# Kernel tuning notes

Measured on AMD Instinct MI355X. Metric: run time of the kernel, lower is better.

## Reference

```python
import jax, jax.numpy as jnp
import numpy as np

N = 10000
E = 160000
H = 8
C = 128
D = 1024
NB = 3
NG = 64
NEG_SLOPE = 0.2
BN_EPS = 1e-5


def setup_inputs() -> dict:
    key = jax.random.key(0)
    ks = jax.random.split(key, 12)
    x = jax.random.normal(ks[0], (N, D), dtype=jnp.float32)
    edge_index = jax.random.randint(ks[1], (2, E), 0, N, dtype=jnp.int64)
    batch = jnp.sort(jax.random.randint(ks[2], (N,), 0, NG, dtype=jnp.int64))
    W = jax.random.normal(ks[3], (NB, D, D), dtype=jnp.float32) * 0.03
    att_src = jax.random.normal(ks[4], (NB, H, C), dtype=jnp.float32) * 0.1
    att_dst = jax.random.normal(ks[5], (NB, H, C), dtype=jnp.float32) * 0.1
    att_bias = jnp.zeros((NB, D), dtype=jnp.float32)
    gamma = jnp.ones((NB, D), dtype=jnp.float32)
    beta = jnp.zeros((NB, D), dtype=jnp.float32)
    W_out = jax.random.normal(ks[6], (D, 2), dtype=jnp.float32) * 0.03
    b_out = jnp.zeros((2,), dtype=jnp.float32)
    return {"x": x, "edge_index": edge_index, "batch": batch, "W": W,
            "att_src": att_src, "att_dst": att_dst, "att_bias": att_bias,
            "gamma": gamma, "beta": beta, "W_out": W_out, "b_out": b_out}


def _gat_conv(x, Wb, a_src, a_dst, bias, src, dst):
    # linear projection, per-head view: [N, H, C]
    h = (x @ Wb).reshape(N, H, C)
    alpha_src = jnp.einsum('nhc,hc->nh', h, a_src)  # [N,H]
    alpha_dst = jnp.einsum('nhc,hc->nh', h, a_dst)
    e = jax.nn.leaky_relu(alpha_src[src] + alpha_dst[dst], NEG_SLOPE)  # [Etot,H]
    # segment softmax over incoming edges per destination node
    m = jax.ops.segment_max(e, dst, num_segments=N)  # every node has self-loop
    ex = jnp.exp(e - m[dst])
    denom = jax.ops.segment_sum(ex, dst, num_segments=N)
    alpha = ex / denom[dst]  # [Etot,H]
    msg = alpha[:, :, None] * h[src]  # [Etot,H,C]
    out = jax.ops.segment_sum(msg, dst, num_segments=N).reshape(N, H * C)
    return out + bias


def _batchnorm(x, g, b):
    mu = jnp.mean(x, axis=0)
    var = jnp.mean(jnp.square(x - mu), axis=0)  # biased, training mode
    return (x - mu) * jax.lax.rsqrt(var + BN_EPS) * g + b


def reference(x, edge_index, batch, W, att_src, att_dst, att_bias, gamma, beta, W_out, b_out):
    # add self loops (PyG GATConv default)
    loop = jnp.arange(N, dtype=edge_index.dtype)
    src = jnp.concatenate([edge_index[0], loop])
    dst = jnp.concatenate([edge_index[1], loop])

    h = x
    prev = x
    for i in range(NB):
        att = _gat_conv(h, W[i], att_src[i], att_dst[i], att_bias[i], src, dst)
        o = jax.nn.relu(_batchnorm(prev + att, gamma[i], beta[i]))
        prev = h
        h = o

    # global mean pool over graphs
    sums = jax.ops.segment_sum(h, batch, num_segments=NG)
    cnts = jax.ops.segment_sum(jnp.ones((N,), dtype=h.dtype), batch, num_segments=NG)
    pooled = sums / jnp.maximum(cnts, 1.0)[:, None]
    return pooled @ W_out + b_out
```

## Files before the change

### kernel.cpp

```cpp
#include <hip/hip_runtime.h>
#include <hip/hip_bf16.h>

#define N_NODES 10000
#define E_EDGES 160000
#define ETOT    170000
#define H_HEADS 8
#define C_CH    128
#define D_DIM   1024
#define NBLK    3
#define NGRAPH  64
#define NEG_SLOPE 0.2f
#define BN_EPS  1e-5f

typedef __attribute__((ext_vector_type(8))) _Float16 half8;
typedef __attribute__((ext_vector_type(4))) _Float16 half4;
typedef __attribute__((ext_vector_type(2))) _Float16 half2v;
typedef __attribute__((ext_vector_type(4))) float f32x4;

__device__ inline int lower_bound_batch(const int* __restrict__ batch, int g) {
    int lo = 0, hi = N_NODES;
    while (lo < hi) {
        int mid = (lo + hi) >> 1;
        if (batch[mid] < g) lo = mid + 1;
        else hi = mid;
    }
    return lo;
}

__global__ void deg_kernel(const int* __restrict__ ei, int* __restrict__ deg) {
    int tid = blockIdx.x * blockDim.x + threadIdx.x;
    if (tid >= ETOT) return;
    int dst = (tid < E_EDGES) ? ei[E_EDGES + tid] : (tid - E_EDGES);
    atomicAdd(&deg[dst], 1);
}

__global__ void scan_kernel(const int* __restrict__ deg, int* __restrict__ ioff) {
    __shared__ int part[256];
    int t = threadIdx.x;
    const int CH = (N_NODES + 255) / 256;
    int base = t * CH;
    int s = 0;
    for (int j = 0; j < CH; ++j) {
        int idx = base + j;
        if (idx < N_NODES) s += deg[idx];
    }
    part[t] = s;
    __syncthreads();
    for (int o = 1; o < 256; o <<= 1) {
        int v = 0;
        if (t >= o) v = part[t - o];
        __syncthreads();
        part[t] += v;
        __syncthreads();
    }
    int run = (t == 0) ? 0 : part[t - 1];
    for (int j = 0; j < CH; ++j) {
        int idx = base + j;
        if (idx < N_NODES) { ioff[idx] = run; run += deg[idx]; }
    }
}

__global__ void scatter_kernel(const int* __restrict__ ei, int* __restrict__ ioff,
                               int* __restrict__ csr_src) {
    int tid = blockIdx.x * blockDim.x + threadIdx.x;
    if (tid >= ETOT) return;
    int src, dst;
    if (tid < E_EDGES) { src = ei[tid]; dst = ei[E_EDGES + tid]; }
    else { src = dst = tid - E_EDGES; }
    int pos = atomicAdd(&ioff[dst], 1);
    csr_src[pos] = src;
}

__global__ __launch_bounds__(256) void xconv_kernel(const float* __restrict__ in,
                                                    _Float16* __restrict__ o, int n4) {
    int i = blockIdx.x * blockDim.x + threadIdx.x;
    if (i >= n4) return;
    float4 v = ((const float4*)in)[i];
    half4 h = {(_Float16)v.x, (_Float16)v.y, (_Float16)v.z, (_Float16)v.w};
    ((half4*)o)[i] = h;
}

__global__ __launch_bounds__(256) void wtconv_kernel(const float* __restrict__ Wall,
                                                     _Float16* __restrict__ t16all) {
    const float* W = Wall + (size_t)blockIdx.z * D_DIM * D_DIM;
    _Float16* t16 = t16all + (size_t)blockIdx.z * D_DIM * D_DIM;
    __shared__ float t[32][33];
    int bn = blockIdx.x * 32;
    int bk = blockIdx.y * 32;
    int tx = threadIdx.x & 31;
    int ty = threadIdx.x >> 5;
#pragma unroll
    for (int r = 0; r < 32; r += 8)
        t[ty + r][tx] = W[(size_t)(bk + ty + r) * D_DIM + bn + tx];
    __syncthreads();
#pragma unroll
    for (int r = 0; r < 32; r += 8)
        t16[(size_t)(bn + ty + r) * D_DIM + bk + tx] = (_Float16)t[tx][ty + r];
}

__global__ __launch_bounds__(256, 4) void gemm_mfma_kernel(const _Float16* __restrict__ A,
                                                           const _Float16* __restrict__ Bt,
                                                           _Float16* __restrict__ Hout,
                                                           const float* __restrict__ att_s,
                                                           const float* __restrict__ att_d,
                                                           float* __restrict__ asrc,
                                                           float* __restrict__ adst,
                                                           float* __restrict__ stats, int M) {
    __shared__ short As[128 * 64];
    __shared__ short Bs[64 * 64];
    int bx = blockIdx.x;
    int tid = threadIdx.x;
    if (bx == 0) {
#pragma unroll
        for (int j = 0; j < 8; ++j) stats[tid + j * 256] = 0.f;
    }
    int c = bx & 7;
    int nt = (bx >> 3) & 15;
    int mt = c + 8 * (bx >> 7);
    if (mt >= 79) return;
    int bm = mt * 128;
    int head = nt >> 1;
    int bncol = (nt & 1) * 64;
    int bnrow = nt * 64;
    int wave = tid >> 6;
    int lane = tid & 63;
    int wm = wave * 32;
    int quad = lane >> 4;
    int l16 = lane & 15;

    f32x4 acc[2][4];
#pragma unroll
    for (int i = 0; i < 2; ++i)
#pragma unroll
        for (int j = 0; j < 4; ++j) acc[i][j] = (f32x4){0.f, 0.f, 0.f, 0.f};

    int srow8 = lane >> 3;
    int sswz = ((lane & 7) ^ srow8) << 4;
    const char* gA[4];
    const char* gB[2];
    char* ldA[4];
    char* ldB[2];
#pragma unroll
    for (int r = 0; r < 4; ++r) {
        int arow = wave * 8 + r * 32 + srow8;
        int ga = bm + arow;
        if (ga > M - 1) ga = M - 1;
        gA[r] = (const char*)(A + (size_t)ga * 1024) + sswz;
        ldA[r] = (char*)As + (wave * 8 + r * 32) * 128;
    }
#pragma unroll
    for (int r = 0; r < 2; ++r) {
        int brow = wave * 8 + r * 32 + srow8;
        gB[r] = (const char*)(Bt + (size_t)(bnrow + brow) * 1024) + sswz;
        ldB[r] = (char*)Bs + (wave * 8 + r * 32) * 128;
    }

    int xr = l16 & 7;
    for (int kb = 0; kb < 16; ++kb) {
        int ko = kb * 128;
#pragma unroll
        for (int r = 0; r < 4; ++r)
            __builtin_amdgcn_global_load_lds(
                (const __attribute__((address_space(1))) void*)(gA[r] + ko),
                (__attribute__((address_space(3))) void*)ldA[r], 16, 0, 0);
#pragma unroll
        for (int r = 0; r < 2; ++r)
            __builtin_amdgcn_global_load_lds(
                (const __attribute__((address_space(1))) void*)(gB[r] + ko),
                (__attribute__((address_space(3))) void*)ldB[r], 16, 0, 0);
        __syncthreads();
#pragma unroll
        for (int h = 0; h < 2; ++h) {
            int sl = (quad + h * 4) ^ xr;
            half8 af[2], bfr[4];
#pragma unroll
            for (int i = 0; i < 2; ++i)
                af[i] = *(const half8*)(As + (wm + i * 16 + l16) * 64 + sl * 8);
#pragma unroll
            for (int j = 0; j < 4; ++j)
                bfr[j] = *(const half8*)(Bs + (j * 16 + l16) * 64 + sl * 8);
#pragma unroll
            for (int i = 0; i < 2; ++i)
#pragma unroll
                for (int j = 0; j < 4; ++j)
                    acc[i][j] = __builtin_amdgcn_mfma_f32_16x16x32_f16(af[i], bfr[j], acc[i][j], 0, 0, 0);
        }
        __syncthreads();
    }

    float wsv[4], wdv[4];
#pragma unroll
    for (int j = 0; j < 4; ++j) {
        int cc = bncol + j * 16 + l16;
        wsv[j] = att_s[head * 128 + cc];
        wdv[j] = att_d[head * 128 + cc];
    }
#pragma unroll
    for (int i = 0; i < 2; ++i) {
#pragma unroll
        for (int reg = 0; reg < 4; ++reg) {
            float p = acc[i][0][reg] * wsv[0] + acc[i][1][reg] * wsv[1] +
                      acc[i][2][reg] * wsv[2] + acc[i][3][reg] * wsv[3];
            float q = acc[i][0][reg] * wdv[0] + acc[i][1][reg] * wdv[1] +
                      acc[i][2][reg] * wdv[2] + acc[i][3][reg] * wdv[3];
#pragma unroll
            for (int o = 1; o < 16; o <<= 1) {
                p += __shfl_xor(p, o);
                q += __shfl_xor(q, o);
            }
            if (l16 == 0) {
                int gr = bm + wm + i * 16 + quad * 4 + reg;
                if (gr < M) {
                    atomicAdd(&asrc[gr * 8 + head], p);
                    atomicAdd(&adst[gr * 8 + head], q);
                }
            }
        }
    }
#pragma unroll
    for (int i = 0; i < 2; ++i) {
#pragma unroll
        for (int reg = 0; reg < 4; ++reg) {
            int gr = bm + wm + i * 16 + quad * 4 + reg;
            if (gr < M) {
                _Float16* hp = Hout + (size_t)head * N_NODES * 128 + (size_t)gr * 128 + bncol + l16;
#pragma unroll
                for (int j = 0; j < 4; ++j) hp[j * 16] = (_Float16)acc[i][j][reg];
            }
        }
    }
}

__global__ __launch_bounds__(256) void agg_kernel(const _Float16* __restrict__ h16,
                                                  const float* __restrict__ asrc,
                                                  const float* __restrict__ adst,
                                                  const int* __restrict__ ioff,
                                                  const int* __restrict__ csr_src,
                                                  const _Float16* __restrict__ prevh,
                                                  const float* __restrict__ bias,
                                                  _Float16* __restrict__ yout) {
    int bx = blockIdx.x;
    int head = bx & 7;
    int wave = threadIdx.x >> 6;
    int lane = threadIdx.x & 63;
    int sub = lane >> 4;
    int l16 = lane & 15;
    unsigned c8 = (unsigned)(l16 * 8);
    int n = (bx >> 3) * 4 + wave;
    const _Float16* hh = h16 + (size_t)head * N_NODES * 128;
    int start = (n == 0) ? 0 : ioff[n - 1];
    int end = ioff[n];
    float ad = adst[(unsigned)n * 8u + (unsigned)head];
    float den = 0.f;
    float acc[8];
#pragma unroll
    for (int j = 0; j < 8; ++j) acc[j] = 0.f;
    for (int p = start + sub; p < end; p += 4) {
        int s = csr_src[p];
        float a = asrc[(unsigned)s * 8u + (unsigned)head];
        half8 hv = *(const half8*)(hh + ((unsigned)s * 128u + c8));
        float e = a + ad;
        e = fmaxf(e, NEG_SLOPE * e);
        float ex = __expf(e);
        den += ex;
#pragma unroll
        for (int j = 0; j < 8; ++j)
            acc[j] = fmaf(ex, (float)hv[j], acc[j]);
    }
#pragma unroll
    for (int j = 0; j < 8; ++j) {
        acc[j] += __shfl_xor(acc[j], 16);
        acc[j] += __shfl_xor(acc[j], 32);
    }
    den += __shfl_xor(den, 16);
    den += __shfl_xor(den, 32);
    if (sub == 0) {
        float invd = 1.0f / den;
        int col = head * 128 + l16 * 8;
        half8 ph = *(const half8*)(prevh + (size_t)n * 1024 + col);
        float4 b0 = *(const float4*)(bias + col);
        float4 b1 = *(const float4*)(bias + col + 4);
        half8 o;
        o[0] = (_Float16)fmaf(acc[0], invd, (float)ph[0] + b0.x);
        o[1] = (_Float16)fmaf(acc[1], invd, (float)ph[1] + b0.y);
        o[2] = (_Float16)fmaf(acc[2], invd, (float)ph[2] + b0.z);
        o[3] = (_Float16)fmaf(acc[3], invd, (float)ph[3] + b0.w);
        o[4] = (_Float16)fmaf(acc[4], invd, (float)ph[4] + b1.x);
        o[5] = (_Float16)fmaf(acc[5], invd, (float)ph[5] + b1.y);
        o[6] = (_Float16)fmaf(acc[6], invd, (float)ph[6] + b1.z);
        o[7] = (_Float16)fmaf(acc[7], invd, (float)ph[7] + b1.w);
        *(half8*)(yout + (size_t)n * 1024 + col) = o;
    }
}

__global__ void bn_stats_kernel(const _Float16* __restrict__ y, float* __restrict__ stats) {
    int col = (blockIdx.x * 256 + threadIdx.x) * 2;
    float s0 = 0.f, s1 = 0.f, q0 = 0.f, q1 = 0.f;
    for (int r = blockIdx.y; r < N_NODES; r += gridDim.y) {
        half2v v = *(const half2v*)(y + (size_t)r * 1024 + col);
        float a = (float)v[0], b = (float)v[1];
        s0 += a; q0 += a * a;
        s1 += b; q1 += b * b;
    }
    atomicAdd(&stats[col], s0);
    atomicAdd(&stats[col + 1], s1);
    atomicAdd(&stats[1024 + col], q0);
    atomicAdd(&stats[1024 + col + 1], q1);
}

__global__ void bn_apply_kernel(const _Float16* __restrict__ y, const float* __restrict__ stats,
                                const float* __restrict__ gamma, const float* __restrict__ beta,
                                _Float16* __restrict__ oout, float* __restrict__ azero) {
    int idx4 = blockIdx.x * blockDim.x + threadIdx.x;
    if (idx4 < 2 * N_NODES * H_HEADS / 4)
        ((float4*)azero)[idx4] = make_float4(0.f, 0.f, 0.f, 0.f);
    if (idx4 >= N_NODES * D_DIM / 4) return;
    int base = idx4 * 4;
    int col = base & 1023;
    const float invN = 1.0f / (float)N_NODES;
    half4 v = ((const half4*)y)[idx4];
    float r[4];
#pragma unroll
    for (int j = 0; j < 4; ++j) {
        int cc = col + j;
        float mu = stats[cc] * invN;
        float var = stats[1024 + cc] * invN - mu * mu;
        float t = ((float)v[j] - mu) * rsqrtf(var + BN_EPS) * gamma[cc] + beta[cc];
        r[j] = fmaxf(t, 0.f);
    }
    half4 h = {(_Float16)r[0], (_Float16)r[1], (_Float16)r[2], (_Float16)r[3]};
    ((half4*)oout)[idx4] = h;
}

__global__ __launch_bounds__(256) void pool_kernel(const _Float16* __restrict__ h3,
                                                   const int* __restrict__ batch,
                                                   float* __restrict__ pooled) {
    int g = blockIdx.y;
    int col = threadIdx.x * 4;
    int lo = lower_bound_batch(batch, g);
    int hi = lower_bound_batch(batch, g + 1);
    int len = hi - lo;
    int r0 = lo + (int)(((long long)len * blockIdx.x) >> 3);
    int r1 = lo + (int)(((long long)len * (blockIdx.x + 1)) >> 3);
    float a0 = 0.f, a1 = 0.f, a2 = 0.f, a3 = 0.f;
    for (int r = r0; r < r1; ++r) {
        half4 v = *(const half4*)(h3 + (size_t)r * 1024 + col);
        a0 += (float)v[0]; a1 += (float)v[1]; a2 += (float)v[2]; a3 += (float)v[3];
    }
    if (r1 > r0) {
        atomicAdd(&pooled[(size_t)g * 1024 + col + 0], a0);
        atomicAdd(&pooled[(size_t)g * 1024 + col + 1], a1);
        atomicAdd(&pooled[(size_t)g * 1024 + col + 2], a2);
        atomicAdd(&pooled[(size_t)g * 1024 + col + 3], a3);
    }
}

__global__ void final_kernel(const float* __restrict__ pooled, const int* __restrict__ batch,
                             const float* __restrict__ Wout, const float* __restrict__ bout,
                             float* __restrict__ out) {
    int g = blockIdx.x;
    int t = threadIdx.x;
    float p0 = 0.f, p1 = 0.f;
    for (int d = t; d < 1024; d += 256) {
        float v = pooled[(size_t)g * 1024 + d];
        p0 = fmaf(v, Wout[2 * d], p0);
        p1 = fmaf(v, Wout[2 * d + 1], p1);
    }
    __shared__ float s0[256], s1[256];
    s0[t] = p0; s1[t] = p1;
    __syncthreads();
    for (int o = 128; o; o >>= 1) {
        if (t < o) { s0[t] += s0[t + o]; s1[t] += s1[t + o]; }
        __syncthreads();
    }
    if (t == 0) {
        int cnt = lower_bound_batch(batch, g + 1) - lower_bound_batch(batch, g);
        float inv = 1.0f / fmaxf((float)cnt, 1.0f);
        out[g * 2 + 0] = s0[0] * inv + bout[0];
        out[g * 2 + 1] = s1[0] * inv + bout[1];
    }
}

extern "C" void kernel_launch(void* const* d_in, const int* in_sizes, int n_in,
                              void* d_out, int out_size, void* d_ws, size_t ws_size,
                              hipStream_t stream) {
    const float* x        = (const float*)d_in[0];
    const int*   ei       = (const int*)d_in[1];
    const int*   batch    = (const int*)d_in[2];
    const float* W        = (const float*)d_in[3];
    const float* att_src  = (const float*)d_in[4];
    const float* att_dst  = (const float*)d_in[5];
    const float* att_bias = (const float*)d_in[6];
    const float* gamma    = (const float*)d_in[7];
    const float* beta     = (const float*)d_in[8];
    const float* Wout     = (const float*)d_in[9];
    const float* bout     = (const float*)d_in[10];
    float* out = (float*)d_out;

    const size_t ND = (size_t)N_NODES * D_DIM;
    float* ws = (float*)d_ws;
    float* asrc   = ws;
    float* adst   = asrc + (size_t)N_NODES * H_HEADS;
    float* stats  = adst + (size_t)N_NODES * H_HEADS;
    float* pooled = stats + 2 * D_DIM;
    int* ideg     = (int*)(pooled + (size_t)NGRAPH * D_DIM);
    int* ioff     = ideg + N_NODES;
    int* csr_src  = ioff + N_NODES;
    _Float16* bufP  = (_Float16*)(csr_src + ETOT);
    _Float16* bufO0 = bufP + ND;
    _Float16* h16   = bufO0 + ND;
    _Float16* y16   = h16 + ND;
    _Float16* Wt3   = y16 + ND;

    hipMemsetAsync(ideg, 0, N_NODES * sizeof(int), stream);
    hipMemsetAsync(pooled, 0, (size_t)NGRAPH * D_DIM * sizeof(float), stream);
    hipMemsetAsync(asrc, 0, (size_t)2 * N_NODES * H_HEADS * sizeof(float), stream);
    deg_kernel<<<(ETOT + 255) / 256, 256, 0, stream>>>(ei, ideg);
    scan_kernel<<<1, 256, 0, stream>>>(ideg, ioff);
    scatter_kernel<<<(ETOT + 255) / 256, 256, 0, stream>>>(ei, ioff, csr_src);
    xconv_kernel<<<(int)(ND / 4 + 255) / 256, 256, 0, stream>>>(x, bufP, (int)(ND / 4));
    wtconv_kernel<<<dim3(32, 32, 3), 256, 0, stream>>>(W, Wt3);

    const _Float16* Ain[3]  = {bufP, bufO0, bufP};
    const _Float16* Pin[3]  = {bufP, bufP, bufO0};
    _Float16* Oout[3]       = {bufO0, bufP, bufP};

    for (int i = 0; i < NBLK; ++i) {
        gemm_mfma_kernel<<<1280, 256, 0, stream>>>(
            Ain[i], Wt3 + (size_t)i * D_DIM * D_DIM, h16,
            att_src + i * H_HEADS * C_CH, att_dst + i * H_HEADS * C_CH,
            asrc, adst, stats, N_NODES);
        agg_kernel<<<(N_NODES / 4) * H_HEADS, 256, 0, stream>>>(
            h16, asrc, adst, ioff, csr_src, Pin[i], att_bias + i * D_DIM, y16);
        bn_stats_kernel<<<dim3(2, 128), 256, 0, stream>>>(y16, stats);
        bn_apply_kernel<<<(int)(ND / 4 + 255) / 256, 256, 0, stream>>>(
            y16, stats, gamma + i * D_DIM, beta + i * D_DIM, Oout[i], asrc);
    }

    pool_kernel<<<dim3(8, NGRAPH), 256, 0, stream>>>(bufP, batch, pooled);
    final_kernel<<<NGRAPH, 256, 0, stream>>>(pooled, batch, Wout, bout, out);
}
```

Before: 593.7 us.

## Precompute per-edge attention exponentials in separate kernel and unroll aggregation loop

Adds an edge_exp_kernel that computes leaky-relu and exp of the attention logits once per CSR edge for all 8 heads, storing them head-major, and a csr_dst array to support it. The aggregation kernel then reads the precomputed weights coalesced instead of gathering asrc per source and evaluating exp itself, and its edge loop is unrolled by two to get more gathers in flight. The cost is an extra kernel launch per block plus writing and reading about 5 MB of edge weights.

```diff
diff --git a/kernel.cpp b/kernel.cpp
--- a/kernel.cpp
+++ b/kernel.cpp
@@ -61,7 +61,7 @@
 }
 
 __global__ void scatter_kernel(const int* __restrict__ ei, int* __restrict__ ioff,
-                               int* __restrict__ csr_src) {
+                               int* __restrict__ csr_src, int* __restrict__ csr_dst) {
     int tid = blockIdx.x * blockDim.x + threadIdx.x;
     if (tid >= ETOT) return;
     int src, dst;
@@ -69,6 +69,7 @@
     else { src = dst = tid - E_EDGES; }
     int pos = atomicAdd(&ioff[dst], 1);
     csr_src[pos] = src;
+    csr_dst[pos] = dst;
 }
 
 __global__ __launch_bounds__(256) void xconv_kernel(const float* __restrict__ in,
@@ -231,9 +232,31 @@
     }
 }
 
+__global__ __launch_bounds__(256) void edge_exp_kernel(const int* __restrict__ csr_src,
+                                                       const int* __restrict__ csr_dst,
+                                                       const float* __restrict__ asrc,
+                                                       const float* __restrict__ adst,
+                                                       float* __restrict__ exw) {
+    int p = blockIdx.x * 256 + threadIdx.x;
+    if (p >= ETOT) return;
+    int s = csr_src[p];
+    int d = csr_dst[p];
+    float4 s0 = *(const float4*)(asrc + (unsigned)s * 8u);
+    float4 s1 = *(const float4*)(asrc + (unsigned)s * 8u + 4u);
+    float4 d0 = *(const float4*)(adst + (unsigned)d * 8u);
+    float4 d1 = *(const float4*)(adst + (unsigned)d * 8u + 4u);
+    float e[8] = {s0.x + d0.x, s0.y + d0.y, s0.z + d0.z, s0.w + d0.w,
+                  s1.x + d1.x, s1.y + d1.y, s1.z + d1.z, s1.w + d1.w};
+#pragma unroll
+    for (int j = 0; j < 8; ++j) {
+        float v = e[j];
+        v = (v > 0.f) ? v : NEG_SLOPE * v;
+        exw[j * ETOT + p] = __expf(v);
+    }
+}
+
 __global__ __launch_bounds__(256) void agg_kernel(const _Float16* __restrict__ h16,
-                                                  const float* __restrict__ asrc,
-                                                  const float* __restrict__ adst,
+                                                  const float* __restrict__ exw,
                                                   const int* __restrict__ ioff,
                                                   const int* __restrict__ csr_src,
                                                   const _Float16* __restrict__ prevh,
@@ -248,24 +271,43 @@
     unsigned c8 = (unsigned)(l16 * 8);
     int n = (bx >> 3) * 4 + wave;
     const _Float16* hh = h16 + (size_t)head * N_NODES * 128;
+    const float* exh = exw + (size_t)head * ETOT;
     int start = (n == 0) ? 0 : ioff[n - 1];
     int end = ioff[n];
-    float ad = adst[(unsigned)n * 8u + (unsigned)head];
     float den = 0.f;
     float acc[8];
 #pragma unroll
     for (int j = 0; j < 8; ++j) acc[j] = 0.f;
-    for (int p = start + sub; p < end; p += 4) {
-        int s = csr_src[p];
-        float a = asrc[(unsigned)s * 8u + (unsigned)head];
+    int p = start;
+    for (; p + 8 <= end; p += 8) {
+        int sA = csr_src[p + sub];
+        int sB = csr_src[p + 4 + sub];
+        float xA = exh[p + sub];
+        float xB = exh[p + 4 + sub];
+        half8 hA = *(const half8*)(hh + ((unsigned)sA * 128u + c8));
+        half8 hB = *(const half8*)(hh + ((unsigned)sB * 128u + c8));
+        den += xA + xB;
+#pragma unroll
+        for (int j = 0; j < 8; ++j)
+            acc[j] = fmaf(xA, (float)hA[j], fmaf(xB, (float)hB[j], acc[j]));
+    }
+    for (; p + 4 <= end; p += 4) {
+        int s = csr_src[p + sub];
+        float x = exh[p + sub];
         half8 hv = *(const half8*)(hh + ((unsigned)s * 128u + c8));
-        float e = a + ad;
-        e = fmaxf(e, NEG_SLOPE * e);
-        float ex = __expf(e);
-        den += ex;
+        den += x;
 #pragma unroll
         for (int j = 0; j < 8; ++j)
-            acc[j] = fmaf(ex, (float)hv[j], acc[j]);
+            acc[j] = fmaf(x, (float)hv[j], acc[j]);
+    }
+    if (p + sub < end) {
+        int s = csr_src[p + sub];
+        float x = exh[p + sub];
+        half8 hv = *(const half8*)(hh + ((unsigned)s * 128u + c8));
+        den += x;
+#pragma unroll
+        for (int j = 0; j < 8; ++j)
+            acc[j] = fmaf(x, (float)hv[j], acc[j]);
     }
 #pragma unroll
     for (int j = 0; j < 8; ++j) {
@@ -406,7 +448,9 @@
     int* ideg     = (int*)(pooled + (size_t)NGRAPH * D_DIM);
     int* ioff     = ideg + N_NODES;
     int* csr_src  = ioff + N_NODES;
-    _Float16* bufP  = (_Float16*)(csr_src + ETOT);
+    int* csr_dst  = csr_src + ETOT;
+    float* exw    = (float*)(csr_dst + ETOT);
+    _Float16* bufP  = (_Float16*)(exw + (size_t)ETOT * H_HEADS);
     _Float16* bufO0 = bufP + ND;
     _Float16* h16   = bufO0 + ND;
     _Float16* y16   = h16 + ND;
@@ -417,7 +461,7 @@
     hipMemsetAsync(asrc, 0, (size_t)2 * N_NODES * H_HEADS * sizeof(float), stream);
     deg_kernel<<<(ETOT + 255) / 256, 256, 0, stream>>>(ei, ideg);
     scan_kernel<<<1, 256, 0, stream>>>(ideg, ioff);
-    scatter_kernel<<<(ETOT + 255) / 256, 256, 0, stream>>>(ei, ioff, csr_src);
+    scatter_kernel<<<(ETOT + 255) / 256, 256, 0, stream>>>(ei, ioff, csr_src, csr_dst);
     xconv_kernel<<<(int)(ND / 4 + 255) / 256, 256, 0, stream>>>(x, bufP, (int)(ND / 4));
     wtconv_kernel<<<dim3(32, 32, 3), 256, 0, stream>>>(W, Wt3);
 
@@ -430,8 +474,10 @@
             Ain[i], Wt3 + (size_t)i * D_DIM * D_DIM, h16,
             att_src + i * H_HEADS * C_CH, att_dst + i * H_HEADS * C_CH,
             asrc, adst, stats, N_NODES);
+        edge_exp_kernel<<<(ETOT + 255) / 256, 256, 0, stream>>>(csr_src, csr_dst,
+                                                                asrc, adst, exw);
         agg_kernel<<<(N_NODES / 4) * H_HEADS, 256, 0, stream>>>(
-            h16, asrc, adst, ioff, csr_src, Pin[i], att_bias + i * D_DIM, y16);
+            h16, exw, ioff, csr_src, Pin[i], att_bias + i * D_DIM, y16);
         bn_stats_kernel<<<dim3(2, 128), 256, 0, stream>>>(y16, stats);
         bn_apply_kernel<<<(int)(ND / 4 + 255) / 256, 256, 0, stream>>>(
             y16, stats, gamma + i * D_DIM, beta + i * D_DIM, Oout[i], asrc);
```

After: 545.6 us (median of 3 runs). 8.1% less time.
